# Optimization experiments

Measured on AMD Instinct MI355X. Metric: run time of the kernel, lower is better.

Reference implementation:

```python
import jax, jax.numpy as jnp
import numpy as np
import math

B, S, D, H = 2, 2048, 1024, 16
HD = D // H

def setup_inputs() -> dict:
    key = jax.random.key(0)
    ks = jax.random.split(key, 12)
    s = 0.02
    inp = {
        'query': jax.random.normal(ks[0], (B, S, D), jnp.float32),
        'key':   jax.random.normal(ks[1], (B, S, D), jnp.float32),
        'value': jax.random.normal(ks[2], (B, S, D), jnp.float32),
        # causal mask: True = masked out
        'mask': jnp.broadcast_to(~jnp.tril(jnp.ones((S, S), bool)), (B, S, S)),
        'Wq': jax.random.normal(ks[3], (D, D), jnp.float32) * s,
        'bq': jnp.zeros((D,), jnp.float32),
        'Wk': jax.random.normal(ks[4], (D, D), jnp.float32) * s,
        'bk': jnp.zeros((D,), jnp.float32),
        'Wv': jax.random.normal(ks[5], (D, D), jnp.float32) * s,
        'bv': jnp.zeros((D,), jnp.float32),
        'Wo': jax.random.normal(ks[6], (D, D), jnp.float32) * s,
        'bo': jnp.zeros((D,), jnp.float32),
    }
    return inp

def reference(query, key, value, mask, Wq, bq, Wk, bk, Wv, bv, Wo, bo):
    def shape(x):  # [B,S,D] -> [B,H,S,HD]
        return x.reshape(B, -1, H, HD).transpose(0, 2, 1, 3)
    Q = shape(query @ Wq.T + bq) / math.sqrt(HD)
    K = shape(key @ Wk.T + bk)
    V = shape(value @ Wv.T + bv)
    scores = jnp.einsum('bhqd,bhkd->bhqk', Q, K).astype(jnp.float32)
    scores = jnp.where(mask[:, None, :, :], -1e18, scores)
    attn = jax.nn.softmax(scores, axis=-1).astype(query.dtype)
    # dropout p=0 (inference)
    ctx = jnp.einsum('bhqk,bhkd->bhqd', attn, V)
    ctx = ctx.transpose(0, 2, 1, 3).reshape(B, -1, D)
    output = ctx @ Wo.T + bo
    return output, attn
```

## Files before the change

### kernel.cpp

```cpp
#include <hip/hip_runtime.h>
#include <hip/hip_fp16.h>

typedef _Float16 f16;
typedef f16 f16x8 __attribute__((ext_vector_type(8)));
typedef float f32x4 __attribute__((ext_vector_type(4)));

#define MFMA16(a, b, c) __builtin_amdgcn_mfma_f32_16x16x32_f16(a, b, c, 0, 0, 0)

static constexpr int Bn = 2, Sn = 2048, Dn = 1024, Hn = 16, HDn = 64;
static constexpr int Mn = Bn * Sn;

__device__ inline void gload_lds16(const void* g, void* l) {
    __builtin_amdgcn_global_load_lds((const __attribute__((address_space(1))) void*)g,
                                     (__attribute__((address_space(3))) void*)l,
                                     16, 0, 0);
}

__device__ inline int swz(int row, int chunk) {
    return row * 64 + ((chunk ^ (row & 7)) * 8);
}

__global__ __launch_bounds__(256) void convert_all(
    const float* __restrict__ q, const float* __restrict__ k, const float* __restrict__ v,
    const float* __restrict__ wq, const float* __restrict__ wk, const float* __restrict__ wv,
    const float* __restrict__ wo,
    f16* qo, f16* ko, f16* vo, f16* wqo, f16* wko, f16* wvo, f16* woo) {
    const int c = blockIdx.x * 256 + threadIdx.x;
    const float* src;
    f16* dst;
    int off;
    if (c < 3 * 524288) {
        const int t = c >> 19;
        off = c & 524287;
        src = (t == 0) ? q : (t == 1) ? k : v;
        dst = (t == 0) ? qo : (t == 1) ? ko : vo;
    } else {
        const int c2 = c - 3 * 524288;
        const int t = c2 >> 17;
        off = c2 & 131071;
        src = (t == 0) ? wq : (t == 1) ? wk : (t == 2) ? wv : wo;
        dst = (t == 0) ? wqo : (t == 1) ? wko : (t == 2) ? wvo : woo;
    }
    const float4 a = ((const float4*)src)[off * 2];
    const float4 b = ((const float4*)src)[off * 2 + 1];
    f16x8 r = {(f16)a.x, (f16)a.y, (f16)a.z, (f16)a.w,
               (f16)b.x, (f16)b.y, (f16)b.z, (f16)b.w};
    *(f16x8*)(dst + (size_t)off * 8) = r;
}

struct GemmArgs {
    const f16* X[3];
    const f16* W[3];
    const float* bias[3];
    void* out[3];
    float scale[3];
    int mode[3];
};

__global__ __launch_bounds__(256) void gemm_qkv(GemmArgs args) {
    __shared__ __align__(16) f16 sbuf[17408];
    f16* As = sbuf;
    f16* Bs = sbuf + 8192;

    const int z = blockIdx.z;
    const f16* __restrict__ X = args.X[z];
    const f16* __restrict__ W = args.W[z];
    const float* __restrict__ bias = args.bias[z];
    const float scale = args.scale[z];
    const int mode = args.mode[z];

    const int tid = threadIdx.x, w = tid >> 6, lane = tid & 63;
    const int lr = lane & 15, lg = lane >> 4;
    const int m0 = blockIdx.y * 128, n0 = blockIdx.x * 128;
    const int wm = (w >> 1) * 64, wn = (w & 1) * 64;

    const int dr = lane >> 3;
    const int schunk = (lane & 7) ^ dr;

    f32x4 acc[4][4] = {};

    for (int k0 = 0; k0 < Dn; k0 += 64) {
        __syncthreads();
#pragma unroll
        for (int j = 0; j < 4; ++j) {
            gload_lds16(X + (size_t)(m0 + w * 32 + j * 8 + dr) * Dn + k0 + schunk * 8,
                        &As[(w * 4 + j) * 512]);
            gload_lds16(W + (size_t)(n0 + w * 32 + j * 8 + dr) * Dn + k0 + schunk * 8,
                        &Bs[(w * 4 + j) * 512]);
        }
        __syncthreads();

#pragma unroll
        for (int half = 0; half < 2; ++half) {
            f16x8 a[4], b[4];
#pragma unroll
            for (int mi = 0; mi < 4; ++mi)
                a[mi] = *(const f16x8*)&As[swz(wm + mi * 16 + lr, half * 4 + lg)];
#pragma unroll
            for (int ni = 0; ni < 4; ++ni)
                b[ni] = *(const f16x8*)&Bs[swz(wn + ni * 16 + lr, half * 4 + lg)];
#pragma unroll
            for (int mi = 0; mi < 4; ++mi)
#pragma unroll
                for (int ni = 0; ni < 4; ++ni)
                    acc[mi][ni] = MFMA16(a[mi], b[ni], acc[mi][ni]);
        }
    }

    float bv[4];
#pragma unroll
    for (int ni = 0; ni < 4; ++ni) bv[ni] = bias[n0 + wn + ni * 16 + lr];

    __syncthreads();
    if (mode == 0) {
#pragma unroll
        for (int mi = 0; mi < 4; ++mi)
#pragma unroll
            for (int ni = 0; ni < 4; ++ni)
#pragma unroll
                for (int j = 0; j < 4; ++j)
                    sbuf[(wm + mi * 16 + lg * 4 + j) * 136 + wn + ni * 16 + lr] =
                        (f16)((acc[mi][ni][j] + bv[ni]) * scale);
        __syncthreads();
        f16* out = (f16*)args.out[z];
#pragma unroll
        for (int t = 0; t < 8; ++t) {
            const int idx = t * 256 + tid;
            const int r = idx >> 4, cc = (idx & 15) * 8;
            *(f16x8*)(out + (size_t)(m0 + r) * Dn + n0 + cc) = *(f16x8*)&sbuf[r * 136 + cc];
        }
    } else {
#pragma unroll
        for (int mi = 0; mi < 4; ++mi)
#pragma unroll
            for (int ni = 0; ni < 4; ++ni)
#pragma unroll
                for (int j = 0; j < 4; ++j)
                    sbuf[(wn + ni * 16 + lr) * 136 + wm + mi * 16 + lg * 4 + j] =
                        (f16)((acc[mi][ni][j] + bv[ni]) * scale);
        __syncthreads();
        f16* out = (f16*)args.out[z];
        const int b = m0 >> 11, s0 = m0 & (Sn - 1);
#pragma unroll
        for (int t = 0; t < 8; ++t) {
            const int idx = t * 256 + tid;
            const int nn = idx >> 4, cc = (idx & 15) * 8;
            const int n = n0 + nn;
            const int hh = n >> 6, d = n & 63;
            *(f16x8*)(out + (((size_t)(b * Hn + hh) * HDn + d) * Sn) + s0 + cc) =
                *(f16x8*)&sbuf[nn * 136 + cc];
        }
    }
}

__global__ __launch_bounds__(512) void flash_ctx(const f16* __restrict__ Qh,
                                                 const f16* __restrict__ Kh,
                                                 const f16* __restrict__ Vt,
                                                 f16* __restrict__ ctx,
                                                 float* __restrict__ rinv_g) {
    __shared__ __align__(16) f16 Qs[8192];
    __shared__ __align__(16) f16 Ks[4096];
    __shared__ __align__(16) f16 Vts[4096];
    __shared__ __align__(16) f16 Ps[8 * 16 * 72];

    const int tid = threadIdx.x, w = tid >> 6, lane = tid & 63;
    const int lr = lane & 15, lg = lane >> 4;
    const int qt = (Sn / 128 - 1) - blockIdx.x;
    const int bh = blockIdx.y;
    const int b = bh >> 4, h = bh & 15;

    const int dr = lane >> 3;
    const int schunk = (lane & 7) ^ dr;

    const f16* Qb = Qh + (size_t)b * Sn * Dn + h * HDn;
    const f16* Kb = Kh + (size_t)b * Sn * Dn + h * HDn;
    const f16* Vtb = Vt + (size_t)bh * HDn * Sn;

#pragma unroll
    for (int i = 0; i < 2; ++i)
        gload_lds16(Qb + (size_t)(qt * 128 + w * 16 + i * 8 + dr) * Dn + schunk * 8,
                    &Qs[(w * 16 + i * 8) * 64]);
    __syncthreads();
    f16x8 qa[2];
#pragma unroll
    for (int kh = 0; kh < 2; ++kh)
        qa[kh] = *(const f16x8*)&Qs[swz(w * 16 + lr, kh * 4 + lg)];

    float lsum[4] = {0.f, 0.f, 0.f, 0.f};
    f32x4 octx[4] = {};
    const int ktmax = 2 * qt + 1;

    for (int kt = 0; kt <= ktmax; ++kt) {
        __syncthreads();
        gload_lds16(Kb + (size_t)(kt * 64 + w * 8 + dr) * Dn + schunk * 8, &Ks[w * 512]);
        gload_lds16(Vtb + (size_t)(w * 8 + dr) * Sn + kt * 64 + schunk * 8, &Vts[w * 512]);
        __syncthreads();

#pragma unroll
        for (int nf = 0; nf < 4; ++nf) {
            f32x4 a = {};
            a = MFMA16(qa[0], *(const f16x8*)&Ks[swz(nf * 16 + lr, lg)], a);
            a = MFMA16(qa[1], *(const f16x8*)&Ks[swz(nf * 16 + lr, 4 + lg)], a);
#pragma unroll
            for (int j = 0; j < 4; ++j) {
                const int qg = qt * 128 + w * 16 + lg * 4 + j;
                const int kg = kt * 64 + nf * 16 + lr;
                const float p = (kg > qg) ? 0.f : __expf(a[j]);
                lsum[j] += p;
                Ps[w * 1152 + (lg * 4 + j) * 72 + nf * 16 + lr] = (f16)p;
            }
        }

        f16x8 pa0 = *(const f16x8*)&Ps[w * 1152 + lr * 72 + lg * 8];
        f16x8 pa1 = *(const f16x8*)&Ps[w * 1152 + lr * 72 + 32 + lg * 8];
#pragma unroll
        for (int df = 0; df < 4; ++df) {
            octx[df] = MFMA16(pa0, *(const f16x8*)&Vts[swz(df * 16 + lr, lg)], octx[df]);
            octx[df] = MFMA16(pa1, *(const f16x8*)&Vts[swz(df * 16 + lr, 4 + lg)], octx[df]);
        }
    }

    float rv[4];
#pragma unroll
    for (int j = 0; j < 4; ++j) {
        float s = lsum[j];
        s += __shfl_xor(s, 1);
        s += __shfl_xor(s, 2);
        s += __shfl_xor(s, 4);
        s += __shfl_xor(s, 8);
        rv[j] = 1.0f / s;
    }

#pragma unroll
    for (int df = 0; df < 4; ++df)
#pragma unroll
        for (int j = 0; j < 4; ++j) {
            const int sq = qt * 128 + w * 16 + lg * 4 + j;
            ctx[((size_t)b * Sn + sq) * Dn + h * HDn + df * 16 + lr] =
                (f16)(octx[df][j] * rv[j]);
        }
    if (lr == 0) {
#pragma unroll
        for (int j = 0; j < 4; ++j)
            rinv_g[(size_t)bh * Sn + qt * 128 + w * 16 + lg * 4 + j] = rv[j];
    }
}

__global__ __launch_bounds__(256) void tail_fused(const f16* __restrict__ Qh,
                                                  const f16* __restrict__ Kh,
                                                  const float* __restrict__ rinv_g,
                                                  float* __restrict__ attn,
                                                  const f16* __restrict__ ctxX,
                                                  const f16* __restrict__ Wo,
                                                  const float* __restrict__ bo,
                                                  float* __restrict__ out_f) {
    __shared__ __align__(16) f16 lds_[16384];

    const int tid = threadIdx.x, w = tid >> 6, lane = tid & 63;
    const int lr = lane & 15, lg = lane >> 4;
    const int dr = lane >> 3;
    const int schunk = (lane & 7) ^ dr;

    if (blockIdx.x < 256) {
        f16* As = lds_;
        f16* Bs = lds_ + 8192;
        const int n0 = (blockIdx.x & 7) * 128, m0 = (blockIdx.x >> 3) * 128;
        const int wm = (w >> 1) * 64, wn = (w & 1) * 64;

        f32x4 acc[4][4] = {};
        for (int k0 = 0; k0 < Dn; k0 += 64) {
            __syncthreads();
#pragma unroll
            for (int j = 0; j < 4; ++j) {
                gload_lds16(ctxX + (size_t)(m0 + w * 32 + j * 8 + dr) * Dn + k0 + schunk * 8,
                            &As[(w * 4 + j) * 512]);
                gload_lds16(Wo + (size_t)(n0 + w * 32 + j * 8 + dr) * Dn + k0 + schunk * 8,
                            &Bs[(w * 4 + j) * 512]);
            }
            __syncthreads();
#pragma unroll
            for (int half = 0; half < 2; ++half) {
                f16x8 a[4], b[4];
#pragma unroll
                for (int mi = 0; mi < 4; ++mi)
                    a[mi] = *(const f16x8*)&As[swz(wm + mi * 16 + lr, half * 4 + lg)];
#pragma unroll
                for (int ni = 0; ni < 4; ++ni)
                    b[ni] = *(const f16x8*)&Bs[swz(wn + ni * 16 + lr, half * 4 + lg)];
#pragma unroll
                for (int mi = 0; mi < 4; ++mi)
#pragma unroll
                    for (int ni = 0; ni < 4; ++ni)
                        acc[mi][ni] = MFMA16(a[mi], b[ni], acc[mi][ni]);
            }
        }
        float bv[4];
#pragma unroll
        for (int ni = 0; ni < 4; ++ni) bv[ni] = bo[n0 + wn + ni * 16 + lr];
#pragma unroll
        for (int mi = 0; mi < 4; ++mi)
#pragma unroll
            for (int ni = 0; ni < 4; ++ni)
#pragma unroll
                for (int j = 0; j < 4; ++j)
                    out_f[(size_t)(m0 + wm + mi * 16 + lg * 4 + j) * Dn + n0 + wn + ni * 16 + lr] =
                        acc[mi][ni][j] + bv[ni];
        return;
    }

    const int bid = blockIdx.x - 256;
    const int qt = 31 - (bid & 31);
    const int bh = bid >> 5;
    const int b = bh >> 4, h = bh & 15;

    f16* Qs = lds_;
    f16* Ks = lds_ + 4096;

    const f16* Qb = Qh + (size_t)b * Sn * Dn + h * HDn;
    const f16* Kb = Kh + (size_t)b * Sn * Dn + h * HDn;
    float* attn_base = attn + ((size_t)bh * Sn + qt * 64) * Sn;

#pragma unroll
    for (int i = 0; i < 2; ++i)
        gload_lds16(Qb + (size_t)(qt * 64 + w * 16 + i * 8 + dr) * Dn + schunk * 8,
                    &Qs[(w * 16 + i * 8) * 64]);

    float rv[4];
#pragma unroll
    for (int j = 0; j < 4; ++j)
        rv[j] = rinv_g[(size_t)bh * Sn + qt * 64 + w * 16 + lg * 4 + j];

    __syncthreads();
    f16x8 qa[2];
#pragma unroll
    for (int kh = 0; kh < 2; ++kh)
        qa[kh] = *(const f16x8*)&Qs[swz(w * 16 + lr, kh * 4 + lg)];

    for (int kt = 0; kt <= qt; ++kt) {
        __syncthreads();
#pragma unroll
        for (int i = 0; i < 2; ++i)
            gload_lds16(Kb + (size_t)(kt * 64 + w * 16 + i * 8 + dr) * Dn + schunk * 8,
                        &Ks[(w * 16 + i * 8) * 64]);
        __syncthreads();

        const bool diag = (kt == qt);
#pragma unroll
        for (int nf = 0; nf < 4; ++nf) {
            f32x4 a = {};
            a = MFMA16(qa[0], *(const f16x8*)&Ks[swz(nf * 16 + lr, lg)], a);
            a = MFMA16(qa[1], *(const f16x8*)&Ks[swz(nf * 16 + lr, 4 + lg)], a);
#pragma unroll
            for (int j = 0; j < 4; ++j) {
                const int qr = w * 16 + lg * 4 + j;
                const int kc = nf * 16 + lr;
                const float p = (diag && kc > qr) ? 0.f : __expf(a[j]) * rv[j];
                attn_base[(size_t)qr * Sn + kt * 64 + kc] = p;
            }
        }
    }

    const int colstart = (qt + 1) * 64;
    const int width4 = (Sn - colstart) >> 2;
    const float4 z = {0.f, 0.f, 0.f, 0.f};
    for (int r = 0; r < 64; ++r) {
        float4* dst = (float4*)(attn_base + (size_t)r * Sn + colstart);
        for (int c = tid; c < width4; c += 256) dst[c] = z;
    }
}

extern "C" void kernel_launch(void* const* d_in, const int* in_sizes, int n_in,
                              void* d_out, int out_size, void* d_ws, size_t ws_size,
                              hipStream_t stream) {
    const float* query = (const float*)d_in[0];
    const float* key   = (const float*)d_in[1];
    const float* value = (const float*)d_in[2];
    const float* Wq = (const float*)d_in[4];
    const float* bq = (const float*)d_in[5];
    const float* Wk = (const float*)d_in[6];
    const float* bk = (const float*)d_in[7];
    const float* Wv = (const float*)d_in[8];
    const float* bv = (const float*)d_in[9];
    const float* Wo = (const float*)d_in[10];
    const float* bo = (const float*)d_in[11];

    const size_t mk = (size_t)Mn * Dn;
    const size_t nk = (size_t)Dn * Dn;
    f16* p = (f16*)d_ws;
    f16 *Xq16 = p, *Xk16 = p + mk, *Xv16 = p + 2 * mk;
    f16 *Wq16 = p + 3 * mk, *Wk16 = Wq16 + nk, *Wv16 = Wq16 + 2 * nk, *Wo16 = Wq16 + 3 * nk;
    f16 *Qh = Wq16 + 4 * nk, *Kh = Qh + mk, *Vt = Qh + 2 * mk, *ctx = Qh + 3 * mk;
    float* rinv_g = (float*)(ctx + mk);

    float* out_f  = (float*)d_out;
    float* attn_f = out_f + (size_t)Bn * Sn * Dn;

    hipLaunchKernelGGL(convert_all, dim3(8192), dim3(256), 0, stream,
                       query, key, value, Wq, Wk, Wv, Wo,
                       Xq16, Xk16, Xv16, Wq16, Wk16, Wv16, Wo16);

    GemmArgs qkv;
    qkv.X[0] = Xq16; qkv.X[1] = Xk16; qkv.X[2] = Xv16;
    qkv.W[0] = Wq16; qkv.W[1] = Wk16; qkv.W[2] = Wv16;
    qkv.bias[0] = bq; qkv.bias[1] = bk; qkv.bias[2] = bv;
    qkv.out[0] = Qh; qkv.out[1] = Kh; qkv.out[2] = Vt;
    qkv.scale[0] = 0.125f; qkv.scale[1] = 1.0f; qkv.scale[2] = 1.0f;
    qkv.mode[0] = 0; qkv.mode[1] = 0; qkv.mode[2] = 1;
    hipLaunchKernelGGL(gemm_qkv, dim3(Dn / 128, Mn / 128, 3), dim3(256), 0, stream, qkv);

    hipLaunchKernelGGL(flash_ctx, dim3(Sn / 128, Bn * Hn), dim3(512), 0, stream,
                       Qh, Kh, Vt, ctx, rinv_g);

    hipLaunchKernelGGL(tail_fused, dim3(256 + 1024), dim3(256), 0, stream,
                       Qh, Kh, rinv_g, attn_f, ctx, Wo16, bo, out_f);
}
```

Measured before the change: 288.9 us.

## Fuse attention-probability writeout into two-pass flash kernel, split out O-projection GEMM

Restructures attention into a two-pass kernel. The first pass over K computes the row sums, and the second pass recomputes scores, normalizes them, accumulates P·V and writes the attention probabilities from the same LDS tile. This removes the separate tail kernel that recomputed QK^T, along with the rinv round-trip through global memory, and the O-projection now runs as its own GEMM launch. In exchange, QK^T is computed twice inside the attention kernel, and the O-projection can no longer overlap with the attention-matrix writes. The probabilities pass through f16 before being written as fp32, which reduces the precision of the stored attention values.

```diff
diff --git a/kernel.cpp b/kernel.cpp
--- a/kernel.cpp
+++ b/kernel.cpp
@@ -153,11 +153,11 @@
     }
 }
 
-__global__ __launch_bounds__(512) void flash_ctx(const f16* __restrict__ Qh,
+__global__ __launch_bounds__(512) void mega_attn(const f16* __restrict__ Qh,
                                                  const f16* __restrict__ Kh,
                                                  const f16* __restrict__ Vt,
                                                  f16* __restrict__ ctx,
-                                                 float* __restrict__ rinv_g) {
+                                                 float* __restrict__ attn) {
     __shared__ __align__(16) f16 Qs[8192];
     __shared__ __align__(16) f16 Ks[4096];
     __shared__ __align__(16) f16 Vts[4096];
@@ -175,6 +175,17 @@
     const f16* Qb = Qh + (size_t)b * Sn * Dn + h * HDn;
     const f16* Kb = Kh + (size_t)b * Sn * Dn + h * HDn;
     const f16* Vtb = Vt + (size_t)bh * HDn * Sn;
+    float* attn_base = attn + ((size_t)bh * Sn + qt * 128) * Sn;
+
+    {
+        const int colstart = (qt + 1) * 128;
+        const int width4 = (Sn - colstart) >> 2;
+        const float4 z = {0.f, 0.f, 0.f, 0.f};
+        for (int r = 0; r < 128; ++r) {
+            float4* dst = (float4*)(attn_base + (size_t)r * Sn + colstart);
+            for (int c = tid; c < width4; c += 512) dst[c] = z;
+        }
+    }
 
 #pragma unroll
     for (int i = 0; i < 2; ++i)
@@ -186,16 +197,13 @@
     for (int kh = 0; kh < 2; ++kh)
         qa[kh] = *(const f16x8*)&Qs[swz(w * 16 + lr, kh * 4 + lg)];
 
+    const int ktmax = 2 * qt + 1;
     float lsum[4] = {0.f, 0.f, 0.f, 0.f};
-    f32x4 octx[4] = {};
-    const int ktmax = 2 * qt + 1;
 
     for (int kt = 0; kt <= ktmax; ++kt) {
         __syncthreads();
         gload_lds16(Kb + (size_t)(kt * 64 + w * 8 + dr) * Dn + schunk * 8, &Ks[w * 512]);
-        gload_lds16(Vtb + (size_t)(w * 8 + dr) * Sn + kt * 64 + schunk * 8, &Vts[w * 512]);
-        __syncthreads();
-
+        __syncthreads();
 #pragma unroll
         for (int nf = 0; nf < 4; ++nf) {
             f32x4 a = {};
@@ -205,18 +213,8 @@
             for (int j = 0; j < 4; ++j) {
                 const int qg = qt * 128 + w * 16 + lg * 4 + j;
                 const int kg = kt * 64 + nf * 16 + lr;
-                const float p = (kg > qg) ? 0.f : __expf(a[j]);
-                lsum[j] += p;
-                Ps[w * 1152 + (lg * 4 + j) * 72 + nf * 16 + lr] = (f16)p;
+                lsum[j] += (kg > qg) ? 0.f : __expf(a[j]);
             }
-        }
-
-        f16x8 pa0 = *(const f16x8*)&Ps[w * 1152 + lr * 72 + lg * 8];
-        f16x8 pa1 = *(const f16x8*)&Ps[w * 1152 + lr * 72 + 32 + lg * 8];
-#pragma unroll
-        for (int df = 0; df < 4; ++df) {
-            octx[df] = MFMA16(pa0, *(const f16x8*)&Vts[swz(df * 16 + lr, lg)], octx[df]);
-            octx[df] = MFMA16(pa1, *(const f16x8*)&Vts[swz(df * 16 + lr, 4 + lg)], octx[df]);
         }
     }
 
@@ -231,120 +229,15 @@
         rv[j] = 1.0f / s;
     }
 
-#pragma unroll
-    for (int df = 0; df < 4; ++df)
-#pragma unroll
-        for (int j = 0; j < 4; ++j) {
-            const int sq = qt * 128 + w * 16 + lg * 4 + j;
-            ctx[((size_t)b * Sn + sq) * Dn + h * HDn + df * 16 + lr] =
-                (f16)(octx[df][j] * rv[j]);
-        }
-    if (lr == 0) {
-#pragma unroll
-        for (int j = 0; j < 4; ++j)
-            rinv_g[(size_t)bh * Sn + qt * 128 + w * 16 + lg * 4 + j] = rv[j];
-    }
-}
-
-__global__ __launch_bounds__(256) void tail_fused(const f16* __restrict__ Qh,
-                                                  const f16* __restrict__ Kh,
-                                                  const float* __restrict__ rinv_g,
-                                                  float* __restrict__ attn,
-                                                  const f16* __restrict__ ctxX,
-                                                  const f16* __restrict__ Wo,
-                                                  const float* __restrict__ bo,
-                                                  float* __restrict__ out_f) {
-    __shared__ __align__(16) f16 lds_[16384];
-
-    const int tid = threadIdx.x, w = tid >> 6, lane = tid & 63;
-    const int lr = lane & 15, lg = lane >> 4;
-    const int dr = lane >> 3;
-    const int schunk = (lane & 7) ^ dr;
-
-    if (blockIdx.x < 256) {
-        f16* As = lds_;
-        f16* Bs = lds_ + 8192;
-        const int n0 = (blockIdx.x & 7) * 128, m0 = (blockIdx.x >> 3) * 128;
-        const int wm = (w >> 1) * 64, wn = (w & 1) * 64;
-
-        f32x4 acc[4][4] = {};
-        for (int k0 = 0; k0 < Dn; k0 += 64) {
-            __syncthreads();
-#pragma unroll
-            for (int j = 0; j < 4; ++j) {
-                gload_lds16(ctxX + (size_t)(m0 + w * 32 + j * 8 + dr) * Dn + k0 + schunk * 8,
-                            &As[(w * 4 + j) * 512]);
-                gload_lds16(Wo + (size_t)(n0 + w * 32 + j * 8 + dr) * Dn + k0 + schunk * 8,
-                            &Bs[(w * 4 + j) * 512]);
-            }
-            __syncthreads();
-#pragma unroll
-            for (int half = 0; half < 2; ++half) {
-                f16x8 a[4], b[4];
-#pragma unroll
-                for (int mi = 0; mi < 4; ++mi)
-                    a[mi] = *(const f16x8*)&As[swz(wm + mi * 16 + lr, half * 4 + lg)];
-#pragma unroll
-                for (int ni = 0; ni < 4; ++ni)
-                    b[ni] = *(const f16x8*)&Bs[swz(wn + ni * 16 + lr, half * 4 + lg)];
-#pragma unroll
-                for (int mi = 0; mi < 4; ++mi)
-#pragma unroll
-                    for (int ni = 0; ni < 4; ++ni)
-                        acc[mi][ni] = MFMA16(a[mi], b[ni], acc[mi][ni]);
-            }
-        }
-        float bv[4];
-#pragma unroll
-        for (int ni = 0; ni < 4; ++ni) bv[ni] = bo[n0 + wn + ni * 16 + lr];
-#pragma unroll
-        for (int mi = 0; mi < 4; ++mi)
-#pragma unroll
-            for (int ni = 0; ni < 4; ++ni)
-#pragma unroll
-                for (int j = 0; j < 4; ++j)
-                    out_f[(size_t)(m0 + wm + mi * 16 + lg * 4 + j) * Dn + n0 + wn + ni * 16 + lr] =
-                        acc[mi][ni][j] + bv[ni];
-        return;
-    }
-
-    const int bid = blockIdx.x - 256;
-    const int qt = 31 - (bid & 31);
-    const int bh = bid >> 5;
-    const int b = bh >> 4, h = bh & 15;
-
-    f16* Qs = lds_;
-    f16* Ks = lds_ + 4096;
-
-    const f16* Qb = Qh + (size_t)b * Sn * Dn + h * HDn;
-    const f16* Kb = Kh + (size_t)b * Sn * Dn + h * HDn;
-    float* attn_base = attn + ((size_t)bh * Sn + qt * 64) * Sn;
-
-#pragma unroll
-    for (int i = 0; i < 2; ++i)
-        gload_lds16(Qb + (size_t)(qt * 64 + w * 16 + i * 8 + dr) * Dn + schunk * 8,
-                    &Qs[(w * 16 + i * 8) * 64]);
-
-    float rv[4];
-#pragma unroll
-    for (int j = 0; j < 4; ++j)
-        rv[j] = rinv_g[(size_t)bh * Sn + qt * 64 + w * 16 + lg * 4 + j];
-
-    __syncthreads();
-    f16x8 qa[2];
-#pragma unroll
-    for (int kh = 0; kh < 2; ++kh)
-        qa[kh] = *(const f16x8*)&Qs[swz(w * 16 + lr, kh * 4 + lg)];
-
-    for (int kt = 0; kt <= qt; ++kt) {
-        __syncthreads();
-#pragma unroll
-        for (int i = 0; i < 2; ++i)
-            gload_lds16(Kb + (size_t)(kt * 64 + w * 16 + i * 8 + dr) * Dn + schunk * 8,
-                        &Ks[(w * 16 + i * 8) * 64]);
-        __syncthreads();
-
-        const bool diag = (kt == qt);
+    f32x4 octx[4] = {};
+    const int rr = lane >> 2, cb = (lane & 3) * 16;
+
+    for (int kt = 0; kt <= ktmax; ++kt) {
+        __syncthreads();
+        gload_lds16(Kb + (size_t)(kt * 64 + w * 8 + dr) * Dn + schunk * 8, &Ks[w * 512]);
+        gload_lds16(Vtb + (size_t)(w * 8 + dr) * Sn + kt * 64 + schunk * 8, &Vts[w * 512]);
+        __syncthreads();
+
 #pragma unroll
         for (int nf = 0; nf < 4; ++nf) {
             f32x4 a = {};
@@ -352,21 +245,98 @@
             a = MFMA16(qa[1], *(const f16x8*)&Ks[swz(nf * 16 + lr, 4 + lg)], a);
 #pragma unroll
             for (int j = 0; j < 4; ++j) {
-                const int qr = w * 16 + lg * 4 + j;
-                const int kc = nf * 16 + lr;
-                const float p = (diag && kc > qr) ? 0.f : __expf(a[j]) * rv[j];
-                attn_base[(size_t)qr * Sn + kt * 64 + kc] = p;
+                const int qg = qt * 128 + w * 16 + lg * 4 + j;
+                const int kg = kt * 64 + nf * 16 + lr;
+                const float p = (kg > qg) ? 0.f : __expf(a[j]) * rv[j];
+                Ps[w * 1152 + (lg * 4 + j) * 72 + nf * 16 + lr] = (f16)p;
             }
         }
-    }
-
-    const int colstart = (qt + 1) * 64;
-    const int width4 = (Sn - colstart) >> 2;
-    const float4 z = {0.f, 0.f, 0.f, 0.f};
-    for (int r = 0; r < 64; ++r) {
-        float4* dst = (float4*)(attn_base + (size_t)r * Sn + colstart);
-        for (int c = tid; c < width4; c += 256) dst[c] = z;
-    }
+
+        f16x8 pa0 = *(const f16x8*)&Ps[w * 1152 + lr * 72 + lg * 8];
+        f16x8 pa1 = *(const f16x8*)&Ps[w * 1152 + lr * 72 + 32 + lg * 8];
+#pragma unroll
+        for (int df = 0; df < 4; ++df) {
+            octx[df] = MFMA16(pa0, *(const f16x8*)&Vts[swz(df * 16 + lr, lg)], octx[df]);
+            octx[df] = MFMA16(pa1, *(const f16x8*)&Vts[swz(df * 16 + lr, 4 + lg)], octx[df]);
+        }
+
+        {
+            f16x8 v0 = *(const f16x8*)&Ps[w * 1152 + rr * 72 + cb];
+            f16x8 v1 = *(const f16x8*)&Ps[w * 1152 + rr * 72 + cb + 8];
+            float* dst = attn_base + (size_t)(w * 16 + rr) * Sn + kt * 64 + cb;
+            float4 o0 = {(float)v0[0], (float)v0[1], (float)v0[2], (float)v0[3]};
+            float4 o1 = {(float)v0[4], (float)v0[5], (float)v0[6], (float)v0[7]};
+            float4 o2 = {(float)v1[0], (float)v1[1], (float)v1[2], (float)v1[3]};
+            float4 o3 = {(float)v1[4], (float)v1[5], (float)v1[6], (float)v1[7]};
+            ((float4*)dst)[0] = o0;
+            ((float4*)dst)[1] = o1;
+            ((float4*)dst)[2] = o2;
+            ((float4*)dst)[3] = o3;
+        }
+    }
+
+#pragma unroll
+    for (int df = 0; df < 4; ++df)
+#pragma unroll
+        for (int j = 0; j < 4; ++j) {
+            const int sq = qt * 128 + w * 16 + lg * 4 + j;
+            ctx[((size_t)b * Sn + sq) * Dn + h * HDn + df * 16 + lr] = (f16)octx[df][j];
+        }
+}
+
+__global__ __launch_bounds__(256) void gemm_oproj(const f16* __restrict__ X,
+                                                  const f16* __restrict__ Wo,
+                                                  const float* __restrict__ bo,
+                                                  float* __restrict__ out_f) {
+    __shared__ __align__(16) f16 sbuf[16384];
+    f16* As = sbuf;
+    f16* Bs = sbuf + 8192;
+
+    const int tid = threadIdx.x, w = tid >> 6, lane = tid & 63;
+    const int lr = lane & 15, lg = lane >> 4;
+    const int n0 = blockIdx.x * 128, m0 = blockIdx.y * 128;
+    const int wm = (w >> 1) * 64, wn = (w & 1) * 64;
+    const int dr = lane >> 3;
+    const int schunk = (lane & 7) ^ dr;
+
+    f32x4 acc[4][4] = {};
+    for (int k0 = 0; k0 < Dn; k0 += 64) {
+        __syncthreads();
+#pragma unroll
+        for (int j = 0; j < 4; ++j) {
+            gload_lds16(X + (size_t)(m0 + w * 32 + j * 8 + dr) * Dn + k0 + schunk * 8,
+                        &As[(w * 4 + j) * 512]);
+            gload_lds16(Wo + (size_t)(n0 + w * 32 + j * 8 + dr) * Dn + k0 + schunk * 8,
+                        &Bs[(w * 4 + j) * 512]);
+        }
+        __syncthreads();
+#pragma unroll
+        for (int half = 0; half < 2; ++half) {
+            f16x8 a[4], b[4];
+#pragma unroll
+            for (int mi = 0; mi < 4; ++mi)
+                a[mi] = *(const f16x8*)&As[swz(wm + mi * 16 + lr, half * 4 + lg)];
+#pragma unroll
+            for (int ni = 0; ni < 4; ++ni)
+                b[ni] = *(const f16x8*)&Bs[swz(wn + ni * 16 + lr, half * 4 + lg)];
+#pragma unroll
+            for (int mi = 0; mi < 4; ++mi)
+#pragma unroll
+                for (int ni = 0; ni < 4; ++ni)
+                    acc[mi][ni] = MFMA16(a[mi], b[ni], acc[mi][ni]);
+        }
+    }
+    float bv[4];
+#pragma unroll
+    for (int ni = 0; ni < 4; ++ni) bv[ni] = bo[n0 + wn + ni * 16 + lr];
+#pragma unroll
+    for (int mi = 0; mi < 4; ++mi)
+#pragma unroll
+        for (int ni = 0; ni < 4; ++ni)
+#pragma unroll
+            for (int j = 0; j < 4; ++j)
+                out_f[(size_t)(m0 + wm + mi * 16 + lg * 4 + j) * Dn + n0 + wn + ni * 16 + lr] =
+                    acc[mi][ni][j] + bv[ni];
 }
 
 extern "C" void kernel_launch(void* const* d_in, const int* in_sizes, int n_in,
@@ -390,7 +360,6 @@
     f16 *Xq16 = p, *Xk16 = p + mk, *Xv16 = p + 2 * mk;
     f16 *Wq16 = p + 3 * mk, *Wk16 = Wq16 + nk, *Wv16 = Wq16 + 2 * nk, *Wo16 = Wq16 + 3 * nk;
     f16 *Qh = Wq16 + 4 * nk, *Kh = Qh + mk, *Vt = Qh + 2 * mk, *ctx = Qh + 3 * mk;
-    float* rinv_g = (float*)(ctx + mk);
 
     float* out_f  = (float*)d_out;
     float* attn_f = out_f + (size_t)Bn * Sn * Dn;
@@ -408,9 +377,9 @@
     qkv.mode[0] = 0; qkv.mode[1] = 0; qkv.mode[2] = 1;
     hipLaunchKernelGGL(gemm_qkv, dim3(Dn / 128, Mn / 128, 3), dim3(256), 0, stream, qkv);
 
-    hipLaunchKernelGGL(flash_ctx, dim3(Sn / 128, Bn * Hn), dim3(512), 0, stream,
-                       Qh, Kh, Vt, ctx, rinv_g);
-
-    hipLaunchKernelGGL(tail_fused, dim3(256 + 1024), dim3(256), 0, stream,
-                       Qh, Kh, rinv_g, attn_f, ctx, Wo16, bo, out_f);
-}
+    hipLaunchKernelGGL(mega_attn, dim3(Sn / 128, Bn * Hn), dim3(512), 0, stream,
+                       Qh, Kh, Vt, ctx, attn_f);
+
+    hipLaunchKernelGGL(gemm_oproj, dim3(Dn / 128, Mn / 128), dim3(256), 0, stream,
+                       ctx, Wo16, bo, out_f);
+}
```

Measured after the change: 312.3 us. 1.08x slower.

## Double-buffer K/V loads in flash and attn kernels; vectorize attn stores via LDS

Applied to the files above, without the earlier changes.

Both the flash context kernel and the attention-probability tail now double-buffer K (and Vt) tiles in LDS. The next tile is prefetched with async global-to-LDS loads while the current one is computed, using explicit vmcnt waits and raw barriers instead of paired __syncthreads. The attn tail also stages probabilities through an LDS scratch tile and writes them to global as contiguous float4 rows, replacing scattered scalar stores. The cost is more LDS per block and hand-tuned waitcnt counts that must match the number of outstanding loads. Staging the probabilities as fp16 also rounds the attn output written to global memory.

```diff
diff --git a/kernel.cpp b/kernel.cpp
--- a/kernel.cpp
+++ b/kernel.cpp
@@ -14,6 +14,19 @@
     __builtin_amdgcn_global_load_lds((const __attribute__((address_space(1))) void*)g,
                                      (__attribute__((address_space(3))) void*)l,
                                      16, 0, 0);
+}
+
+template <int N> __device__ inline void vmwait() {
+    if constexpr (N == 0) asm volatile("s_waitcnt vmcnt(0)" ::: "memory");
+    else if constexpr (N == 2) asm volatile("s_waitcnt vmcnt(2)" ::: "memory");
+    else if constexpr (N == 4) asm volatile("s_waitcnt vmcnt(4)" ::: "memory");
+    else if constexpr (N == 6) asm volatile("s_waitcnt vmcnt(6)" ::: "memory");
+}
+__device__ inline void lgkm0() { asm volatile("s_waitcnt lgkmcnt(0)" ::: "memory"); }
+__device__ inline void barrier() {
+    asm volatile("" ::: "memory");
+    __builtin_amdgcn_s_barrier();
+    asm volatile("" ::: "memory");
 }
 
 __device__ inline int swz(int row, int chunk) {
@@ -159,9 +172,9 @@
                                                  f16* __restrict__ ctx,
                                                  float* __restrict__ rinv_g) {
     __shared__ __align__(16) f16 Qs[8192];
-    __shared__ __align__(16) f16 Ks[4096];
-    __shared__ __align__(16) f16 Vts[4096];
-    __shared__ __align__(16) f16 Ps[8 * 16 * 72];
+    __shared__ __align__(16) f16 Ks[2][4096];
+    __shared__ __align__(16) f16 Vts[2][4096];
+    __shared__ __align__(16) f16 Ps[8 * 1152];
 
     const int tid = threadIdx.x, w = tid >> 6, lane = tid & 63;
     const int lr = lane & 15, lg = lane >> 4;
@@ -176,31 +189,42 @@
     const f16* Kb = Kh + (size_t)b * Sn * Dn + h * HDn;
     const f16* Vtb = Vt + (size_t)bh * HDn * Sn;
 
+    const int ktmax = 2 * qt + 1;
+
 #pragma unroll
     for (int i = 0; i < 2; ++i)
         gload_lds16(Qb + (size_t)(qt * 128 + w * 16 + i * 8 + dr) * Dn + schunk * 8,
                     &Qs[(w * 16 + i * 8) * 64]);
-    __syncthreads();
-    f16x8 qa[2];
-#pragma unroll
-    for (int kh = 0; kh < 2; ++kh)
-        qa[kh] = *(const f16x8*)&Qs[swz(w * 16 + lr, kh * 4 + lg)];
+    gload_lds16(Kb + (size_t)(w * 8 + dr) * Dn + schunk * 8, &Ks[0][w * 512]);
+    gload_lds16(Vtb + (size_t)(w * 8 + dr) * Sn + schunk * 8, &Vts[0][w * 512]);
+    vmwait<2>();
+    barrier();
+    f16x8 qa0 = *(const f16x8*)&Qs[swz(w * 16 + lr, lg)];
+    f16x8 qa1 = *(const f16x8*)&Qs[swz(w * 16 + lr, 4 + lg)];
 
     float lsum[4] = {0.f, 0.f, 0.f, 0.f};
     f32x4 octx[4] = {};
-    const int ktmax = 2 * qt + 1;
 
     for (int kt = 0; kt <= ktmax; ++kt) {
-        __syncthreads();
-        gload_lds16(Kb + (size_t)(kt * 64 + w * 8 + dr) * Dn + schunk * 8, &Ks[w * 512]);
-        gload_lds16(Vtb + (size_t)(w * 8 + dr) * Sn + kt * 64 + schunk * 8, &Vts[w * 512]);
-        __syncthreads();
+        const int cur = kt & 1;
+        lgkm0();
+        barrier();
+        if (kt < ktmax) {
+            gload_lds16(Kb + (size_t)((kt + 1) * 64 + w * 8 + dr) * Dn + schunk * 8,
+                        &Ks[cur ^ 1][w * 512]);
+            gload_lds16(Vtb + (size_t)(w * 8 + dr) * Sn + (kt + 1) * 64 + schunk * 8,
+                        &Vts[cur ^ 1][w * 512]);
+            vmwait<2>();
+        } else {
+            vmwait<0>();
+        }
+        barrier();
 
 #pragma unroll
         for (int nf = 0; nf < 4; ++nf) {
             f32x4 a = {};
-            a = MFMA16(qa[0], *(const f16x8*)&Ks[swz(nf * 16 + lr, lg)], a);
-            a = MFMA16(qa[1], *(const f16x8*)&Ks[swz(nf * 16 + lr, 4 + lg)], a);
+            a = MFMA16(qa0, *(const f16x8*)&Ks[cur][swz(nf * 16 + lr, lg)], a);
+            a = MFMA16(qa1, *(const f16x8*)&Ks[cur][swz(nf * 16 + lr, 4 + lg)], a);
 #pragma unroll
             for (int j = 0; j < 4; ++j) {
                 const int qg = qt * 128 + w * 16 + lg * 4 + j;
@@ -215,8 +239,8 @@
         f16x8 pa1 = *(const f16x8*)&Ps[w * 1152 + lr * 72 + 32 + lg * 8];
 #pragma unroll
         for (int df = 0; df < 4; ++df) {
-            octx[df] = MFMA16(pa0, *(const f16x8*)&Vts[swz(df * 16 + lr, lg)], octx[df]);
-            octx[df] = MFMA16(pa1, *(const f16x8*)&Vts[swz(df * 16 + lr, 4 + lg)], octx[df]);
+            octx[df] = MFMA16(pa0, *(const f16x8*)&Vts[cur][swz(df * 16 + lr, lg)], octx[df]);
+            octx[df] = MFMA16(pa1, *(const f16x8*)&Vts[cur][swz(df * 16 + lr, 4 + lg)], octx[df]);
         }
     }
 
@@ -254,7 +278,7 @@
                                                   const f16* __restrict__ Wo,
                                                   const float* __restrict__ bo,
                                                   float* __restrict__ out_f) {
-    __shared__ __align__(16) f16 lds_[16384];
+    __shared__ __align__(16) f16 lds_[16896];
 
     const int tid = threadIdx.x, w = tid >> 6, lane = tid & 63;
     const int lr = lane & 15, lg = lane >> 4;
@@ -314,49 +338,79 @@
     const int b = bh >> 4, h = bh & 15;
 
     f16* Qs = lds_;
-    f16* Ks = lds_ + 4096;
+    f16* KsA = lds_ + 4096;
+    f16* KsB = lds_ + 8192;
+    f16* Psw = lds_ + 12288;
 
     const f16* Qb = Qh + (size_t)b * Sn * Dn + h * HDn;
     const f16* Kb = Kh + (size_t)b * Sn * Dn + h * HDn;
     float* attn_base = attn + ((size_t)bh * Sn + qt * 64) * Sn;
 
+    float rv[4];
+#pragma unroll
+    for (int j = 0; j < 4; ++j)
+        rv[j] = rinv_g[(size_t)bh * Sn + qt * 64 + w * 16 + lg * 4 + j];
 #pragma unroll
     for (int i = 0; i < 2; ++i)
         gload_lds16(Qb + (size_t)(qt * 64 + w * 16 + i * 8 + dr) * Dn + schunk * 8,
                     &Qs[(w * 16 + i * 8) * 64]);
-
-    float rv[4];
-#pragma unroll
-    for (int j = 0; j < 4; ++j)
-        rv[j] = rinv_g[(size_t)bh * Sn + qt * 64 + w * 16 + lg * 4 + j];
-
-    __syncthreads();
-    f16x8 qa[2];
-#pragma unroll
-    for (int kh = 0; kh < 2; ++kh)
-        qa[kh] = *(const f16x8*)&Qs[swz(w * 16 + lr, kh * 4 + lg)];
+#pragma unroll
+    for (int i = 0; i < 2; ++i)
+        gload_lds16(Kb + (size_t)(w * 16 + i * 8 + dr) * Dn + schunk * 8,
+                    &KsA[(w * 16 + i * 8) * 64]);
+    vmwait<2>();
+    asm volatile("" :: "v"(rv[0]), "v"(rv[1]), "v"(rv[2]), "v"(rv[3]));
+    barrier();
+    f16x8 qa0 = *(const f16x8*)&Qs[swz(w * 16 + lr, lg)];
+    f16x8 qa1 = *(const f16x8*)&Qs[swz(w * 16 + lr, 4 + lg)];
+
+    const int rr = lane >> 2, cb = (lane & 3) * 16;
 
     for (int kt = 0; kt <= qt; ++kt) {
-        __syncthreads();
-#pragma unroll
-        for (int i = 0; i < 2; ++i)
-            gload_lds16(Kb + (size_t)(kt * 64 + w * 16 + i * 8 + dr) * Dn + schunk * 8,
-                        &Ks[(w * 16 + i * 8) * 64]);
-        __syncthreads();
+        f16* Kc = (kt & 1) ? KsB : KsA;
+        f16* Kn = (kt & 1) ? KsA : KsB;
+        lgkm0();
+        barrier();
+        if (kt < qt) {
+#pragma unroll
+            for (int i = 0; i < 2; ++i)
+                gload_lds16(Kb + (size_t)((kt + 1) * 64 + w * 16 + i * 8 + dr) * Dn + schunk * 8,
+                            &Kn[(w * 16 + i * 8) * 64]);
+        }
+        if (kt == 0) {
+            if (kt < qt) vmwait<2>(); else vmwait<0>();
+        } else {
+            if (kt < qt) vmwait<6>(); else vmwait<4>();
+        }
+        barrier();
 
         const bool diag = (kt == qt);
 #pragma unroll
         for (int nf = 0; nf < 4; ++nf) {
             f32x4 a = {};
-            a = MFMA16(qa[0], *(const f16x8*)&Ks[swz(nf * 16 + lr, lg)], a);
-            a = MFMA16(qa[1], *(const f16x8*)&Ks[swz(nf * 16 + lr, 4 + lg)], a);
+            a = MFMA16(qa0, *(const f16x8*)&Kc[swz(nf * 16 + lr, lg)], a);
+            a = MFMA16(qa1, *(const f16x8*)&Kc[swz(nf * 16 + lr, 4 + lg)], a);
 #pragma unroll
             for (int j = 0; j < 4; ++j) {
                 const int qr = w * 16 + lg * 4 + j;
                 const int kc = nf * 16 + lr;
                 const float p = (diag && kc > qr) ? 0.f : __expf(a[j]) * rv[j];
-                attn_base[(size_t)qr * Sn + kt * 64 + kc] = p;
+                Psw[w * 1152 + (lg * 4 + j) * 72 + nf * 16 + lr] = (f16)p;
             }
+        }
+
+        {
+            f16x8 v0 = *(const f16x8*)&Psw[w * 1152 + rr * 72 + cb];
+            f16x8 v1 = *(const f16x8*)&Psw[w * 1152 + rr * 72 + cb + 8];
+            float* dst = attn_base + (size_t)(w * 16 + rr) * Sn + kt * 64 + cb;
+            float4 o0 = {(float)v0[0], (float)v0[1], (float)v0[2], (float)v0[3]};
+            float4 o1 = {(float)v0[4], (float)v0[5], (float)v0[6], (float)v0[7]};
+            float4 o2 = {(float)v1[0], (float)v1[1], (float)v1[2], (float)v1[3]};
+            float4 o3 = {(float)v1[4], (float)v1[5], (float)v1[6], (float)v1[7]};
+            ((float4*)dst)[0] = o0;
+            ((float4*)dst)[1] = o1;
+            ((float4*)dst)[2] = o2;
+            ((float4*)dst)[3] = o3;
         }
     }
 
```

New measurement: 307.5 us. +6.4%, slower.

## Transpose QK MFMA, fold log2e into Q scale, skip masked tiles, vectorize attn stores

Applied to the files above, without the earlier changes.

Swaps the MFMA operand order so each lane holds four consecutive key columns for one query row. This lets probabilities be written as float4 to the attention output and as f16x4 to LDS, and it reduces the row-sum to a single scalar per lane. The log2(e) factor is folded into the Q projection scale so the kernels can call the hardware exp2 directly. Fully masked 16-column fragments skip their MFMA and exp work, and fully unmasked fragments skip the per-element mask compare. The attention writes change from strided scalar stores to 16-byte vector stores, which should cut store instruction count and improve coalescing in the bandwidth-heavy tail kernel.

```diff
diff --git a/kernel.cpp b/kernel.cpp
--- a/kernel.cpp
+++ b/kernel.cpp
@@ -2,6 +2,7 @@
 #include <hip/hip_fp16.h>
 
 typedef _Float16 f16;
+typedef f16 f16x4 __attribute__((ext_vector_type(4)));
 typedef f16 f16x8 __attribute__((ext_vector_type(8)));
 typedef float f32x4 __attribute__((ext_vector_type(4)));
 
@@ -9,6 +10,7 @@
 
 static constexpr int Bn = 2, Sn = 2048, Dn = 1024, Hn = 16, HDn = 64;
 static constexpr int Mn = Bn * Sn;
+static constexpr float kQScale = 0.125f * 1.44269504088896f;
 
 __device__ inline void gload_lds16(const void* g, void* l) {
     __builtin_amdgcn_global_load_lds((const __attribute__((address_space(1))) void*)g,
@@ -161,7 +163,7 @@
     __shared__ __align__(16) f16 Qs[8192];
     __shared__ __align__(16) f16 Ks[4096];
     __shared__ __align__(16) f16 Vts[4096];
-    __shared__ __align__(16) f16 Ps[8 * 16 * 72];
+    __shared__ __align__(16) f16 Ps[8 * 1152];
 
     const int tid = threadIdx.x, w = tid >> 6, lane = tid & 63;
     const int lr = lane & 15, lg = lane >> 4;
@@ -181,12 +183,12 @@
         gload_lds16(Qb + (size_t)(qt * 128 + w * 16 + i * 8 + dr) * Dn + schunk * 8,
                     &Qs[(w * 16 + i * 8) * 64]);
     __syncthreads();
-    f16x8 qa[2];
-#pragma unroll
-    for (int kh = 0; kh < 2; ++kh)
-        qa[kh] = *(const f16x8*)&Qs[swz(w * 16 + lr, kh * 4 + lg)];
-
-    float lsum[4] = {0.f, 0.f, 0.f, 0.f};
+    f16x8 qa0 = *(const f16x8*)&Qs[swz(w * 16 + lr, lg)];
+    f16x8 qa1 = *(const f16x8*)&Qs[swz(w * 16 + lr, 4 + lg)];
+
+    const int qg = qt * 128 + w * 16 + lr;
+    const int qgmin = qt * 128 + w * 16;
+    float lsum = 0.f;
     f32x4 octx[4] = {};
     const int ktmax = 2 * qt + 1;
 
@@ -198,17 +200,30 @@
 
 #pragma unroll
         for (int nf = 0; nf < 4; ++nf) {
+            const int kbase = kt * 64 + nf * 16;
+            f16x4* pdst = (f16x4*)&Ps[w * 1152 + lr * 72 + nf * 16 + lg * 4];
+            if (kbase > qgmin + 15) {
+                *pdst = (f16x4){(f16)0.f, (f16)0.f, (f16)0.f, (f16)0.f};
+                continue;
+            }
+            f16x8 kb0 = *(const f16x8*)&Ks[swz(nf * 16 + lr, lg)];
+            f16x8 kb1 = *(const f16x8*)&Ks[swz(nf * 16 + lr, 4 + lg)];
             f32x4 a = {};
-            a = MFMA16(qa[0], *(const f16x8*)&Ks[swz(nf * 16 + lr, lg)], a);
-            a = MFMA16(qa[1], *(const f16x8*)&Ks[swz(nf * 16 + lr, 4 + lg)], a);
-#pragma unroll
-            for (int j = 0; j < 4; ++j) {
-                const int qg = qt * 128 + w * 16 + lg * 4 + j;
-                const int kg = kt * 64 + nf * 16 + lr;
-                const float p = (kg > qg) ? 0.f : __expf(a[j]);
-                lsum[j] += p;
-                Ps[w * 1152 + (lg * 4 + j) * 72 + nf * 16 + lr] = (f16)p;
-            }
+            a = MFMA16(kb0, qa0, a);
+            a = MFMA16(kb1, qa1, a);
+            float p[4];
+            if (kbase + 15 <= qgmin) {
+#pragma unroll
+                for (int j = 0; j < 4; ++j) p[j] = __builtin_amdgcn_exp2f(a[j]);
+            } else {
+#pragma unroll
+                for (int j = 0; j < 4; ++j) {
+                    const int kg = kbase + lg * 4 + j;
+                    p[j] = (kg > qg) ? 0.f : __builtin_amdgcn_exp2f(a[j]);
+                }
+            }
+            lsum += (p[0] + p[1]) + (p[2] + p[3]);
+            *pdst = (f16x4){(f16)p[0], (f16)p[1], (f16)p[2], (f16)p[3]};
         }
 
         f16x8 pa0 = *(const f16x8*)&Ps[w * 1152 + lr * 72 + lg * 8];
@@ -220,16 +235,16 @@
         }
     }
 
-    float rv[4];
-#pragma unroll
-    for (int j = 0; j < 4; ++j) {
-        float s = lsum[j];
-        s += __shfl_xor(s, 1);
-        s += __shfl_xor(s, 2);
-        s += __shfl_xor(s, 4);
-        s += __shfl_xor(s, 8);
-        rv[j] = 1.0f / s;
-    }
+    lsum += __shfl_xor(lsum, 16);
+    lsum += __shfl_xor(lsum, 32);
+    const float rv = 1.0f / lsum;
+
+    if (lg == 0)
+        rinv_g[(size_t)bh * Sn + qt * 128 + w * 16 + lr] = rv;
+
+    float rvj[4];
+#pragma unroll
+    for (int j = 0; j < 4; ++j) rvj[j] = __shfl(rv, lg * 4 + j);
 
 #pragma unroll
     for (int df = 0; df < 4; ++df)
@@ -237,13 +252,8 @@
         for (int j = 0; j < 4; ++j) {
             const int sq = qt * 128 + w * 16 + lg * 4 + j;
             ctx[((size_t)b * Sn + sq) * Dn + h * HDn + df * 16 + lr] =
-                (f16)(octx[df][j] * rv[j]);
-        }
-    if (lr == 0) {
-#pragma unroll
-        for (int j = 0; j < 4; ++j)
-            rinv_g[(size_t)bh * Sn + qt * 128 + w * 16 + lg * 4 + j] = rv[j];
-    }
+                (f16)(octx[df][j] * rvj[j]);
+        }
 }
 
 __global__ __launch_bounds__(256) void tail_fused(const f16* __restrict__ Qh,
@@ -320,21 +330,19 @@
     const f16* Kb = Kh + (size_t)b * Sn * Dn + h * HDn;
     float* attn_base = attn + ((size_t)bh * Sn + qt * 64) * Sn;
 
+    const float rv = rinv_g[(size_t)bh * Sn + qt * 64 + w * 16 + lr];
+    const int qg = qt * 64 + w * 16 + lr;
+    const int qgmin = qt * 64 + w * 16;
+
 #pragma unroll
     for (int i = 0; i < 2; ++i)
         gload_lds16(Qb + (size_t)(qt * 64 + w * 16 + i * 8 + dr) * Dn + schunk * 8,
                     &Qs[(w * 16 + i * 8) * 64]);
-
-    float rv[4];
-#pragma unroll
-    for (int j = 0; j < 4; ++j)
-        rv[j] = rinv_g[(size_t)bh * Sn + qt * 64 + w * 16 + lg * 4 + j];
-
     __syncthreads();
-    f16x8 qa[2];
-#pragma unroll
-    for (int kh = 0; kh < 2; ++kh)
-        qa[kh] = *(const f16x8*)&Qs[swz(w * 16 + lr, kh * 4 + lg)];
+    f16x8 qa0 = *(const f16x8*)&Qs[swz(w * 16 + lr, lg)];
+    f16x8 qa1 = *(const f16x8*)&Qs[swz(w * 16 + lr, 4 + lg)];
+
+    float* rowp = attn_base + (size_t)(w * 16 + lr) * Sn + lg * 4;
 
     for (int kt = 0; kt <= qt; ++kt) {
         __syncthreads();
@@ -344,19 +352,33 @@
                         &Ks[(w * 16 + i * 8) * 64]);
         __syncthreads();
 
-        const bool diag = (kt == qt);
 #pragma unroll
         for (int nf = 0; nf < 4; ++nf) {
+            const int kbase = kt * 64 + nf * 16;
+            float4* dst = (float4*)(rowp + kbase);
+            if (kbase > qgmin + 15) {
+                *dst = (float4){0.f, 0.f, 0.f, 0.f};
+                continue;
+            }
+            f16x8 kb0 = *(const f16x8*)&Ks[swz(nf * 16 + lr, lg)];
+            f16x8 kb1 = *(const f16x8*)&Ks[swz(nf * 16 + lr, 4 + lg)];
             f32x4 a = {};
-            a = MFMA16(qa[0], *(const f16x8*)&Ks[swz(nf * 16 + lr, lg)], a);
-            a = MFMA16(qa[1], *(const f16x8*)&Ks[swz(nf * 16 + lr, 4 + lg)], a);
-#pragma unroll
-            for (int j = 0; j < 4; ++j) {
-                const int qr = w * 16 + lg * 4 + j;
-                const int kc = nf * 16 + lr;
-                const float p = (diag && kc > qr) ? 0.f : __expf(a[j]) * rv[j];
-                attn_base[(size_t)qr * Sn + kt * 64 + kc] = p;
-            }
+            a = MFMA16(kb0, qa0, a);
+            a = MFMA16(kb1, qa1, a);
+            float4 o;
+            if (kbase + 15 <= qgmin) {
+                o.x = __builtin_amdgcn_exp2f(a[0]) * rv;
+                o.y = __builtin_amdgcn_exp2f(a[1]) * rv;
+                o.z = __builtin_amdgcn_exp2f(a[2]) * rv;
+                o.w = __builtin_amdgcn_exp2f(a[3]) * rv;
+            } else {
+                const int k0g = kbase + lg * 4;
+                o.x = (k0g + 0 > qg) ? 0.f : __builtin_amdgcn_exp2f(a[0]) * rv;
+                o.y = (k0g + 1 > qg) ? 0.f : __builtin_amdgcn_exp2f(a[1]) * rv;
+                o.z = (k0g + 2 > qg) ? 0.f : __builtin_amdgcn_exp2f(a[2]) * rv;
+                o.w = (k0g + 3 > qg) ? 0.f : __builtin_amdgcn_exp2f(a[3]) * rv;
+            }
+            *dst = o;
         }
     }
 
@@ -404,7 +426,7 @@
     qkv.W[0] = Wq16; qkv.W[1] = Wk16; qkv.W[2] = Wv16;
     qkv.bias[0] = bq; qkv.bias[1] = bk; qkv.bias[2] = bv;
     qkv.out[0] = Qh; qkv.out[1] = Kh; qkv.out[2] = Vt;
-    qkv.scale[0] = 0.125f; qkv.scale[1] = 1.0f; qkv.scale[2] = 1.0f;
+    qkv.scale[0] = kQScale; qkv.scale[1] = 1.0f; qkv.scale[2] = 1.0f;
     qkv.mode[0] = 0; qkv.mode[1] = 0; qkv.mode[2] = 1;
     hipLaunchKernelGGL(gemm_qkv, dim3(Dn / 128, Mn / 128, 3), dim3(256), 0, stream, qkv);
 
```

Result: slower. 297.8 us (+3.1%).
